# Kernel tuning notes

Hardware: AMD Instinct MI355X
Metric: run time of the kernel (lower is better)

Reference implementation:

```python
import jax, jax.numpy as jnp
import numpy as np

N_QUBITS = 6
N_LAYERS = 2
SHORT_W = 64
LONG_W = 256
BATCH = 16384


def setup_inputs() -> dict:
    key = jax.random.key(0)
    ks = jax.random.split(key, 15)
    d = {}
    d['xs'] = jax.random.normal(ks[0], (BATCH, 1, SHORT_W), jnp.float32)
    d['xl'] = jax.random.normal(ks[1], (BATCH, 1, LONG_W), jnp.float32)
    d['conv_s_w'] = jax.random.normal(ks[2], (16, 1, 3), jnp.float32) * 0.3
    d['conv_s_b'] = jax.random.normal(ks[3], (16,), jnp.float32) * 0.1
    d['lin_s_w'] = jax.random.normal(ks[4], (N_QUBITS, 16 * SHORT_W), jnp.float32) * 0.03
    d['lin_s_b'] = jax.random.normal(ks[5], (N_QUBITS,), jnp.float32) * 0.1
    d['conv_l_w'] = jax.random.normal(ks[6], (16, 1, 5), jnp.float32) * 0.3
    d['conv_l_b'] = jax.random.normal(ks[7], (16,), jnp.float32) * 0.1
    d['lin_l_w'] = jax.random.normal(ks[8], (N_QUBITS, 16 * LONG_W // 2), jnp.float32) * 0.02
    d['lin_l_b'] = jax.random.normal(ks[9], (N_QUBITS,), jnp.float32) * 0.1
    d['q_weights'] = jax.random.normal(ks[10], (N_LAYERS, N_QUBITS, 3), jnp.float32)
    d['fc1_w'] = jax.random.normal(ks[11], (8, N_QUBITS), jnp.float32) * 0.3
    d['fc1_b'] = jax.random.normal(ks[12], (8,), jnp.float32) * 0.1
    d['fc2_w'] = jax.random.normal(ks[13], (1, 8), jnp.float32) * 0.3
    d['fc2_b'] = jax.random.normal(ks[14], (1,), jnp.float32) * 0.1
    return d


def _conv1d(x, w, b, pad):
    # x: [B,C,W], w: [O,I,K]
    y = jax.lax.conv_general_dilated(x, w, (1,), [(pad, pad)],
                                     dimension_numbers=('NCH', 'OIH', 'NCH'))
    return y + b[None, :, None]


def _apply_1q(state, gate, wire):
    # state: [B,2,2,2,2,2,2]; gate: [2,2] (shared) or [B,2,2] (per-sample)
    s = jnp.moveaxis(state, wire + 1, -1)
    if gate.ndim == 2:
        s = jnp.einsum('...a,ca->...c', s, gate)
    else:
        s = jnp.einsum('b...a,bca->b...c', s, gate)
    return jnp.moveaxis(s, -1, wire + 1)


def _cnot(state, c, t):
    ax_c, ax_t = c + 1, t + 1
    s0 = jnp.take(state, 0, axis=ax_c)
    s1 = jnp.take(state, 1, axis=ax_c)
    t_ax = ax_t - 1 if ax_t > ax_c else ax_t
    s1 = jnp.flip(s1, axis=t_ax)  # X on target when control=1
    return jnp.stack([s0, s1], axis=ax_c)


def _rot(phi, theta, omega):
    # PennyLane Rot = RZ(omega) @ RY(theta) @ RZ(phi)
    c, s = jnp.cos(theta / 2), jnp.sin(theta / 2)
    ep = jnp.exp(-0.5j * (phi + omega).astype(jnp.complex64))
    em = jnp.exp(-0.5j * (phi - omega).astype(jnp.complex64))
    return jnp.array([[0j, 0j], [0j, 0j]]) + jnp.stack([
        jnp.stack([ep * c, -jnp.conj(em) * s]),
        jnp.stack([em * s, jnp.conj(ep) * c])])


def _quantum(f, qw):
    # f: [B, n_qubits] angles-features; qw: [L, n, 3]
    B, n = f.shape
    state = jnp.zeros((B,) + (2,) * n, jnp.complex64)
    state = state.at[(slice(None),) + (0,) * n].set(1.0)
    # RY(pi * f_j) encoding, per-sample gates
    theta = (jnp.pi * f) / 2
    c, s = jnp.cos(theta), jnp.sin(theta)  # [B,n]
    for j in range(n):
        g = jnp.stack([jnp.stack([c[:, j], -s[:, j]], -1),
                       jnp.stack([s[:, j], c[:, j]], -1)], -2).astype(jnp.complex64)
        state = _apply_1q(state, g, j)
    # StronglyEntanglingLayers: Rot on each wire, then CNOT ring with range r
    L = qw.shape[0]
    for l in range(L):
        for j in range(n):
            g = _rot(qw[l, j, 0], qw[l, j, 1], qw[l, j, 2]).astype(jnp.complex64)
            state = _apply_1q(state, g, j)
        r = l % (n - 1) + 1
        for j in range(n):
            state = _cnot(state, j, (j + r) % n)
    # <Z_k> expectations from probabilities
    p = jnp.real(state * jnp.conj(state))  # [B,2,...,2]
    outs = []
    for k in range(n):
        axes = tuple(a for a in range(1, n + 1) if a != k + 1)
        marg = jnp.sum(p, axis=axes)  # [B,2]
        outs.append(marg[:, 0] - marg[:, 1])
    return jnp.stack(outs, axis=-1).astype(jnp.float32)


def reference(xs, xl, conv_s_w, conv_s_b, lin_s_w, lin_s_b,
              conv_l_w, conv_l_b, lin_l_w, lin_l_b,
              q_weights, fc1_w, fc1_b, fc2_w, fc2_b):
    B = xs.shape[0]
    # short branch: Conv1d(1,16,3,pad=1) -> ReLU -> Flatten -> Linear
    hs = jax.nn.relu(_conv1d(xs, conv_s_w, conv_s_b, 1))  # [B,16,SHORT_W]
    fs = hs.reshape(B, -1) @ lin_s_w.T + lin_s_b          # [B,6]
    # long branch: Conv1d(1,16,5,pad=2) -> ReLU -> MaxPool(2) -> Flatten -> Linear
    hl = jax.nn.relu(_conv1d(xl, conv_l_w, conv_l_b, 2))  # [B,16,LONG_W]
    hl = hl.reshape(B, 16, hl.shape[-1] // 2, 2).max(-1)  # MaxPool1d(2)
    fl = hl.reshape(B, -1) @ lin_l_w.T + lin_l_b          # [B,6]
    f = (fs + fl) / 2
    # quantum layer runs on detached values in the original (no grad flow)
    q = _quantum(jax.lax.stop_gradient(f), jax.lax.stop_gradient(q_weights))
    h = jax.nn.relu(q @ fc1_w.T + fc1_b)
    return h @ fc2_w.T + fc2_b  # [B,1]
```

## Files before the change

kernel.cpp:

```cpp
#include <hip/hip_runtime.h>
#include <math.h>

#define SPW 2
#define WAVES_PER_BLOCK 4

#define DPPQ(a,b,c,d) ((a)|((b)<<2)|((c)<<4)|((d)<<6))
#define DPP_XOR1 DPPQ(1,0,3,2)
#define DPP_XOR2 DPPQ(2,3,0,1)
#define DPP_MIR7 0x141
#define DPP_MIR15 0x140

template<int CTRL>
__device__ __forceinline__ float dppf(float v) {
    return __int_as_float(__builtin_amdgcn_update_dpp(
        0, __float_as_int(v), CTRL, 0xF, 0xF, true));
}
template<int OFF>
__device__ __forceinline__ float swzf(float v) {
    return __int_as_float(__builtin_amdgcn_ds_swizzle(__float_as_int(v), OFF));
}
#define SWZ_XOR4  0x101F
#define SWZ_XOR8  0x201F
#define SWZ_XOR16 0x401F

__device__ __forceinline__ float fxor(float v, int s) {
    return __int_as_float(__float_as_int(v) ^ s);
}

__device__ __forceinline__ float wave_bcast_sum(float v) {
    v += dppf<DPP_XOR1>(v);
    v += dppf<DPP_XOR2>(v);
    v += dppf<DPP_MIR7>(v);
    v += dppf<DPP_MIR15>(v);
    v += swzf<SWZ_XOR16>(v);
    v += __shfl_xor(v, 32, 64);
    return v;
}

template<int J> __device__ __forceinline__ float gsh(float v) {
    if constexpr (J == 0) return __shfl_xor(v, 32, 64);
    else if constexpr (J == 1) return swzf<SWZ_XOR16>(v);
    else if constexpr (J == 2) return swzf<SWZ_XOR8>(v);
    else if constexpr (J == 3) return swzf<SWZ_XOR4>(v);
    else if constexpr (J == 4) return dppf<DPP_XOR2>(v);
    else return dppf<DPP_XOR1>(v);
}

__global__ __launch_bounds__(256) void hybridqrc_kernel(
    const float* __restrict__ xs,  const float* __restrict__ xl,
    const float* __restrict__ csw, const float* __restrict__ csb,
    const float* __restrict__ lsw, const float* __restrict__ lsb,
    const float* __restrict__ clw, const float* __restrict__ clb,
    const float* __restrict__ llw, const float* __restrict__ llb,
    const float* __restrict__ qw,  const float* __restrict__ fc1w,
    const float* __restrict__ fc1b,const float* __restrict__ fc2w,
    const float* __restrict__ fc2b,float* __restrict__ out, int B)
{
    __shared__ float4 gme[24];
    const int tid = threadIdx.x;
    if (tid < 24) {
        int g = tid >> 1, bit = tid & 1;
        float phi = qw[g * 3 + 0], th = qw[g * 3 + 1], om = qw[g * 3 + 2];
        float a = 0.5f * (phi + om), b = 0.5f * (phi - om);
        float ca = cosf(a), sa = sinf(a);
        float cb = cosf(b), sb = sinf(b);
        float ct = cosf(0.5f * th), st = sinf(0.5f * th);
        float4 v;
        if (bit) { v.x = ca * ct; v.y =  sa * ct; v.z =  cb * st; v.w = -sb * st; }
        else     { v.x = ca * ct; v.y = -sa * ct; v.z = -cb * st; v.w = -sb * st; }
        gme[tid] = v;
    }
    __syncthreads();

    const int lane = tid & 63;
    const int wave = blockIdx.x * WAVES_PER_BLOCK + (tid >> 6);
    const int base = wave * SPW;
    if (base >= B) return;

    int perm0, perm1;
    {
        int y = lane;
#pragma unroll
        for (int j = 5; j >= 0; j--) {
            const int t = (j + 1) % 6;
            y ^= (y & (1 << (5 - j))) ? (1 << (5 - t)) : 0;
        }
        perm0 = y;
        y = lane;
#pragma unroll
        for (int j = 5; j >= 0; j--) {
            const int t = (j + 2) % 6;
            y ^= (y & (1 << (5 - j))) ? (1 << (5 - t)) : 0;
        }
        perm1 = y;
    }
    int sg[6];
#pragma unroll
    for (int s = 0; s < 6; s++) sg[s] = ((lane >> s) & 1) << 31;

    float acc[SPW][6];
#pragma unroll
    for (int i = 0; i < SPW; i++)
#pragma unroll
        for (int q = 0; q < 6; q++) acc[i][q] = 0.f;

    float xsv[SPW], xm1[SPW], xp1[SPW];
#pragma unroll
    for (int i = 0; i < SPW; i++) xsv[i] = xs[(base + i) * 64 + lane];
#pragma unroll
    for (int i = 0; i < SPW; i++) {
        float lft = __shfl(xsv[i], (lane + 63) & 63, 64);
        float rgt = __shfl(xsv[i], (lane + 1) & 63, 64);
        xm1[i] = (lane == 0)  ? 0.f : lft;
        xp1[i] = (lane == 63) ? 0.f : rgt;
    }
#pragma unroll
    for (int c = 0; c < 16; c++) {
        float w0 = csw[c * 3 + 0], w1 = csw[c * 3 + 1], w2 = csw[c * 3 + 2];
        float bb = csb[c];
        float h[SPW];
#pragma unroll
        for (int i = 0; i < SPW; i++)
            h[i] = fmaxf(0.f, fmaf(w0, xm1[i], fmaf(w1, xsv[i], fmaf(w2, xp1[i], bb))));
#pragma unroll
        for (int q = 0; q < 6; q++) {
            float wv = lsw[q * 1024 + c * 64 + lane];
#pragma unroll
            for (int i = 0; i < SPW; i++) acc[i][q] = fmaf(h[i], wv, acc[i][q]);
        }
    }

    float4 xlv[SPW];
    float l2v[SPW], l1v[SPW], r1v[SPW], r2v[SPW];
#pragma unroll
    for (int i = 0; i < SPW; i++)
        xlv[i] = reinterpret_cast<const float4*>(xl + (size_t)(base + i) * 256)[lane];
#pragma unroll
    for (int i = 0; i < SPW; i++) {
        float a = __shfl(xlv[i].z, (lane + 63) & 63, 64);
        float b = __shfl(xlv[i].w, (lane + 63) & 63, 64);
        float c = __shfl(xlv[i].x, (lane + 1) & 63, 64);
        float d = __shfl(xlv[i].y, (lane + 1) & 63, 64);
        l2v[i] = (lane == 0)  ? 0.f : a;
        l1v[i] = (lane == 0)  ? 0.f : b;
        r1v[i] = (lane == 63) ? 0.f : c;
        r2v[i] = (lane == 63) ? 0.f : d;
    }
#pragma unroll
    for (int c = 0; c < 16; c++) {
        float w0 = clw[c * 5 + 0], w1 = clw[c * 5 + 1], w2 = clw[c * 5 + 2];
        float w3 = clw[c * 5 + 3], w4 = clw[c * 5 + 4];
        float bb = clb[c];
        float p0[SPW], p1[SPW];
#pragma unroll
        for (int i = 0; i < SPW; i++) {
            float vx = xlv[i].x, vy = xlv[i].y, vz = xlv[i].z, vw = xlv[i].w;
            float h0 = fmaf(w0, l2v[i], fmaf(w1, l1v[i], fmaf(w2, vx, fmaf(w3, vy, fmaf(w4, vz, bb)))));
            float h1 = fmaf(w0, l1v[i], fmaf(w1, vx, fmaf(w2, vy, fmaf(w3, vz, fmaf(w4, vw, bb)))));
            float h2 = fmaf(w0, vx, fmaf(w1, vy, fmaf(w2, vz, fmaf(w3, vw, fmaf(w4, r1v[i], bb)))));
            float h3 = fmaf(w0, vy, fmaf(w1, vz, fmaf(w2, vw, fmaf(w3, r1v[i], fmaf(w4, r2v[i], bb)))));
            h0 = fmaxf(h0, 0.f); h1 = fmaxf(h1, 0.f);
            h2 = fmaxf(h2, 0.f); h3 = fmaxf(h3, 0.f);
            p0[i] = fmaxf(h0, h1);
            p1[i] = fmaxf(h2, h3);
        }
#pragma unroll
        for (int q = 0; q < 6; q++) {
            float2 wv = reinterpret_cast<const float2*>(llw + q * 2048 + c * 128)[lane];
#pragma unroll
            for (int i = 0; i < SPW; i++)
                acc[i][q] = fmaf(p0[i], wv.x, fmaf(p1[i], wv.y, acc[i][q]));
        }
    }

    float f[SPW][6];
#pragma unroll
    for (int i = 0; i < SPW; i++)
#pragma unroll
        for (int q = 0; q < 6; q++)
            f[i][q] = 0.5f * (wave_bcast_sum(acc[i][q]) + lsb[q] + llb[q]);

    float ar[SPW], ai[SPW];
#pragma unroll
    for (int i = 0; i < SPW; i++) { ar[i] = 1.f; ai[i] = 0.f; }
#pragma unroll
    for (int j = 0; j < 6; j++) {
        const int mask = 1 << (5 - j);
#pragma unroll
        for (int i = 0; i < SPW; i++) {
            float th = 1.57079632679489662f * f[i][j];
            float ss = __sinf(th), cc = __cosf(th);
            ar[i] *= (lane & mask) ? ss : cc;
        }
    }

#define APPLY_GATE(L, J) do {                                              \
        const int _mask = 1 << (5 - (J));                                  \
        const int _bit = (lane & _mask) ? 1 : 0;                           \
        float4 g = gme[((L) * 6 + (J)) * 2 + _bit];                        \
        _Pragma("unroll")                                                  \
        for (int i = 0; i < SPW; i++) {                                    \
            float br = gsh<J>(ar[i]);                                      \
            float bi = gsh<J>(ai[i]);                                      \
            float nr = g.x * ar[i] - g.y * ai[i] + g.z * br - g.w * bi;    \
            float ni = g.x * ai[i] + g.y * ar[i] + g.z * bi + g.w * br;    \
            ar[i] = nr; ai[i] = ni;                                        \
        } } while (0)

    APPLY_GATE(0, 0); APPLY_GATE(0, 1); APPLY_GATE(0, 2);
    APPLY_GATE(0, 3); APPLY_GATE(0, 4); APPLY_GATE(0, 5);
#pragma unroll
    for (int i = 0; i < SPW; i++) {
        float pr = __shfl(ar[i], perm0, 64);
        float pi2 = __shfl(ai[i], perm0, 64);
        ar[i] = pr; ai[i] = pi2;
    }
    APPLY_GATE(1, 0); APPLY_GATE(1, 1); APPLY_GATE(1, 2);
    APPLY_GATE(1, 3); APPLY_GATE(1, 4); APPLY_GATE(1, 5);
#pragma unroll
    for (int i = 0; i < SPW; i++) {
        float pr = __shfl(ar[i], perm1, 64);
        float pi2 = __shfl(ai[i], perm1, 64);
        ar[i] = pr; ai[i] = pi2;
    }

    float outv[SPW];
#pragma unroll
    for (int i = 0; i < SPW; i++) {
        float v = ar[i] * ar[i] + ai[i] * ai[i];
        float t;
        t = dppf<DPP_XOR1>(v);     v = t + fxor(v, sg[0]);
        t = dppf<DPP_XOR2>(v);     v = t + fxor(v, sg[1]);
        t = swzf<SWZ_XOR4>(v);     v = t + fxor(v, sg[2]);
        t = swzf<SWZ_XOR8>(v);     v = t + fxor(v, sg[3]);
        t = swzf<SWZ_XOR16>(v);    v = t + fxor(v, sg[4]);
        t = __shfl_xor(v, 32, 64); v = t + fxor(v, sg[5]);
        float z[6];
#pragma unroll
        for (int k = 0; k < 6; k++)
            z[k] = __int_as_float(__builtin_amdgcn_readlane(__float_as_int(v), 32 >> k));
        float o = fc2b[0];
#pragma unroll
        for (int m = 0; m < 8; m++) {
            float h = fc1b[m];
#pragma unroll
            for (int k = 0; k < 6; k++) h = fmaf(fc1w[m * 6 + k], z[k], h);
            h = fmaxf(h, 0.f);
            o = fmaf(fc2w[m], h, o);
        }
        outv[i] = o;
    }

    if (lane == 0) {
#pragma unroll
        for (int i = 0; i < SPW; i++)
            if (base + i < B) out[base + i] = outv[i];
    }
}

extern "C" void kernel_launch(void* const* d_in, const int* in_sizes, int n_in,
                              void* d_out, int out_size, void* d_ws, size_t ws_size,
                              hipStream_t stream) {
    const float* xs   = (const float*)d_in[0];
    const float* xl   = (const float*)d_in[1];
    const float* csw  = (const float*)d_in[2];
    const float* csb  = (const float*)d_in[3];
    const float* lsw  = (const float*)d_in[4];
    const float* lsb  = (const float*)d_in[5];
    const float* clw  = (const float*)d_in[6];
    const float* clb  = (const float*)d_in[7];
    const float* llw  = (const float*)d_in[8];
    const float* llb  = (const float*)d_in[9];
    const float* qw   = (const float*)d_in[10];
    const float* fc1w = (const float*)d_in[11];
    const float* fc1b = (const float*)d_in[12];
    const float* fc2w = (const float*)d_in[13];
    const float* fc2b = (const float*)d_in[14];
    float* out = (float*)d_out;

    const int B = in_sizes[0] / 64;
    const int waves = (B + SPW - 1) / SPW;
    const int blocks = (waves + WAVES_PER_BLOCK - 1) / WAVES_PER_BLOCK;
    hybridqrc_kernel<<<blocks, 256, 0, stream>>>(
        xs, xl, csw, csb, lsw, lsb, clw, clb, llw, llb,
        qw, fc1w, fc1b, fc2w, fc2b, out, B);
}
```

Baseline: 123.7 us.

## Stage long-branch linear weights in LDS, use transpose-style multi-value reduction

Each 512-thread block copies the 48 KB long-branch linear weight matrix into shared memory once, and the inner loop reads weights from there instead of global memory. The twelve per-wave sum reductions are replaced by a recursive-halving butterfly that reduces all twelve values together, and the results are gathered with readlane. The DPP and ds_swizzle helpers are replaced by plain __shfl_xor for the gate pairing and the sign-flip marginal reduction. The large LDS footprint and per-block staging cost may limit occupancy. Generic shuffles may also be slower than the DPP forms they replace.

```diff
diff --git a/kernel.cpp b/kernel.cpp
--- a/kernel.cpp
+++ b/kernel.cpp
@@ -2,51 +2,10 @@
 #include <math.h>
 
 #define SPW 2
-#define WAVES_PER_BLOCK 4
-
-#define DPPQ(a,b,c,d) ((a)|((b)<<2)|((c)<<4)|((d)<<6))
-#define DPP_XOR1 DPPQ(1,0,3,2)
-#define DPP_XOR2 DPPQ(2,3,0,1)
-#define DPP_MIR7 0x141
-#define DPP_MIR15 0x140
-
-template<int CTRL>
-__device__ __forceinline__ float dppf(float v) {
-    return __int_as_float(__builtin_amdgcn_update_dpp(
-        0, __float_as_int(v), CTRL, 0xF, 0xF, true));
-}
-template<int OFF>
-__device__ __forceinline__ float swzf(float v) {
-    return __int_as_float(__builtin_amdgcn_ds_swizzle(__float_as_int(v), OFF));
-}
-#define SWZ_XOR4  0x101F
-#define SWZ_XOR8  0x201F
-#define SWZ_XOR16 0x401F
-
-__device__ __forceinline__ float fxor(float v, int s) {
-    return __int_as_float(__float_as_int(v) ^ s);
-}
-
-__device__ __forceinline__ float wave_bcast_sum(float v) {
-    v += dppf<DPP_XOR1>(v);
-    v += dppf<DPP_XOR2>(v);
-    v += dppf<DPP_MIR7>(v);
-    v += dppf<DPP_MIR15>(v);
-    v += swzf<SWZ_XOR16>(v);
-    v += __shfl_xor(v, 32, 64);
-    return v;
-}
-
-template<int J> __device__ __forceinline__ float gsh(float v) {
-    if constexpr (J == 0) return __shfl_xor(v, 32, 64);
-    else if constexpr (J == 1) return swzf<SWZ_XOR16>(v);
-    else if constexpr (J == 2) return swzf<SWZ_XOR8>(v);
-    else if constexpr (J == 3) return swzf<SWZ_XOR4>(v);
-    else if constexpr (J == 4) return dppf<DPP_XOR2>(v);
-    else return dppf<DPP_XOR1>(v);
-}
-
-__global__ __launch_bounds__(256) void hybridqrc_kernel(
+#define WPB 8
+#define NTHR (WPB * 64)
+
+__global__ __launch_bounds__(NTHR) void hybridqrc_kernel(
     const float* __restrict__ xs,  const float* __restrict__ xl,
     const float* __restrict__ csw, const float* __restrict__ csb,
     const float* __restrict__ lsw, const float* __restrict__ lsb,
@@ -56,8 +15,16 @@
     const float* __restrict__ fc1b,const float* __restrict__ fc2w,
     const float* __restrict__ fc2b,float* __restrict__ out, int B)
 {
+    __shared__ float llw_s[12288];
     __shared__ float4 gme[24];
     const int tid = threadIdx.x;
+#pragma unroll
+    for (int idx = 0; idx < 3072; idx += NTHR) {
+        int k = idx + tid;
+        if (k < 3072)
+            reinterpret_cast<float4*>(llw_s)[k] =
+                reinterpret_cast<const float4*>(llw)[k];
+    }
     if (tid < 24) {
         int g = tid >> 1, bit = tid & 1;
         float phi = qw[g * 3 + 0], th = qw[g * 3 + 1], om = qw[g * 3 + 2];
@@ -73,7 +40,7 @@
     __syncthreads();
 
     const int lane = tid & 63;
-    const int wave = blockIdx.x * WAVES_PER_BLOCK + (tid >> 6);
+    const int wave = blockIdx.x * WPB + (tid >> 6);
     const int base = wave * SPW;
     if (base >= B) return;
 
@@ -94,9 +61,6 @@
         }
         perm1 = y;
     }
-    int sg[6];
-#pragma unroll
-    for (int s = 0; s < 6; s++) sg[s] = ((lane >> s) & 1) << 31;
 
     float acc[SPW][6];
 #pragma unroll
@@ -166,19 +130,71 @@
         }
 #pragma unroll
         for (int q = 0; q < 6; q++) {
-            float2 wv = reinterpret_cast<const float2*>(llw + q * 2048 + c * 128)[lane];
+            float2 wv = reinterpret_cast<const float2*>(llw_s + q * 2048 + c * 128)[lane];
 #pragma unroll
             for (int i = 0; i < SPW; i++)
                 acc[i][q] = fmaf(p0[i], wv.x, fmaf(p1[i], wv.y, acc[i][q]));
         }
     }
 
+    float fv[12];
+    {
+        float v[16];
+#pragma unroll
+        for (int q = 0; q < 6; q++) { v[q] = acc[0][q]; v[6 + q] = acc[1][q]; }
+        v[12] = 0.f; v[13] = 0.f; v[14] = 0.f; v[15] = 0.f;
+        {
+            const bool hi = lane & 1;
+#pragma unroll
+            for (int j = 0; j < 8; j++) {
+                float snd = hi ? v[j] : v[j + 8];
+                float rcv = __shfl_xor(snd, 1, 64);
+                float kept = hi ? v[j + 8] : v[j];
+                v[j] = kept + rcv;
+            }
+        }
+        {
+            const bool hi = lane & 2;
+#pragma unroll
+            for (int j = 0; j < 4; j++) {
+                float snd = hi ? v[j] : v[j + 4];
+                float rcv = __shfl_xor(snd, 2, 64);
+                float kept = hi ? v[j + 4] : v[j];
+                v[j] = kept + rcv;
+            }
+        }
+        {
+            const bool hi = lane & 4;
+#pragma unroll
+            for (int j = 0; j < 2; j++) {
+                float snd = hi ? v[j] : v[j + 2];
+                float rcv = __shfl_xor(snd, 4, 64);
+                float kept = hi ? v[j + 2] : v[j];
+                v[j] = kept + rcv;
+            }
+        }
+        {
+            const bool hi = lane & 8;
+            float snd = hi ? v[0] : v[1];
+            float rcv = __shfl_xor(snd, 8, 64);
+            float kept = hi ? v[1] : v[0];
+            v[0] = kept + rcv;
+        }
+        float r = v[0];
+        r += __shfl_xor(r, 16, 64);
+        r += __shfl_xor(r, 32, 64);
+        const int rl[12] = {0, 8, 4, 12, 2, 10, 6, 14, 1, 9, 5, 13};
+#pragma unroll
+        for (int j = 0; j < 12; j++)
+            fv[j] = __int_as_float(
+                __builtin_amdgcn_readlane(__float_as_int(r), rl[j]));
+    }
     float f[SPW][6];
 #pragma unroll
     for (int i = 0; i < SPW; i++)
 #pragma unroll
         for (int q = 0; q < 6; q++)
-            f[i][q] = 0.5f * (wave_bcast_sum(acc[i][q]) + lsb[q] + llb[q]);
+            f[i][q] = 0.5f * (fv[i * 6 + q] + lsb[q] + llb[q]);
 
     float ar[SPW], ai[SPW];
 #pragma unroll
@@ -200,8 +216,8 @@
         float4 g = gme[((L) * 6 + (J)) * 2 + _bit];                        \
         _Pragma("unroll")                                                  \
         for (int i = 0; i < SPW; i++) {                                    \
-            float br = gsh<J>(ar[i]);                                      \
-            float bi = gsh<J>(ai[i]);                                      \
+            float br = __shfl_xor(ar[i], _mask, 64);                       \
+            float bi = __shfl_xor(ai[i], _mask, 64);                       \
             float nr = g.x * ar[i] - g.y * ai[i] + g.z * br - g.w * bi;    \
             float ni = g.x * ai[i] + g.y * ar[i] + g.z * bi + g.w * br;    \
             ar[i] = nr; ai[i] = ni;                                        \
@@ -228,17 +244,16 @@
 #pragma unroll
     for (int i = 0; i < SPW; i++) {
         float v = ar[i] * ar[i] + ai[i] * ai[i];
-        float t;
-        t = dppf<DPP_XOR1>(v);     v = t + fxor(v, sg[0]);
-        t = dppf<DPP_XOR2>(v);     v = t + fxor(v, sg[1]);
-        t = swzf<SWZ_XOR4>(v);     v = t + fxor(v, sg[2]);
-        t = swzf<SWZ_XOR8>(v);     v = t + fxor(v, sg[3]);
-        t = swzf<SWZ_XOR16>(v);    v = t + fxor(v, sg[4]);
-        t = __shfl_xor(v, 32, 64); v = t + fxor(v, sg[5]);
+#pragma unroll
+        for (int m = 1; m < 64; m <<= 1) {
+            float pp = __shfl_xor(v, m, 64);
+            v = (lane & m) ? (pp - v) : (v + pp);
+        }
         float z[6];
 #pragma unroll
         for (int k = 0; k < 6; k++)
-            z[k] = __int_as_float(__builtin_amdgcn_readlane(__float_as_int(v), 32 >> k));
+            z[k] = __int_as_float(
+                __builtin_amdgcn_readlane(__float_as_int(v), 32 >> k));
         float o = fc2b[0];
 #pragma unroll
         for (int m = 0; m < 8; m++) {
@@ -279,9 +294,9 @@
     float* out = (float*)d_out;
 
     const int B = in_sizes[0] / 64;
-    const int waves = (B + SPW - 1) / SPW;
-    const int blocks = (waves + WAVES_PER_BLOCK - 1) / WAVES_PER_BLOCK;
-    hybridqrc_kernel<<<blocks, 256, 0, stream>>>(
+    const int spb = WPB * SPW;
+    const int blocks = (B + spb - 1) / spb;
+    hybridqrc_kernel<<<blocks, NTHR, 0, stream>>>(
         xs, xl, csw, csb, lsw, lsb, clw, clb, llw, llb,
         qw, fc1w, fc1b, fc2w, fc2b, out, B);
 }
```

Result: faster. 116.9 us (-5.5%).
